# Kernel tuning notes

Measured on AMD Instinct MI355X. Metric: run time of the kernel, lower is better.

Reference implementation:

```python
import jax, jax.numpy as jnp
import numpy as np

N_HEADS = 4
D_HEAD = 32  # out_features // n_heads = 128 // 4
NEG_SLOPE = 0.2


def setup_inputs() -> dict:
    key = jax.random.key(0)
    k_x, k_adj, k_w, k_a = jax.random.split(key, 4)
    B, N, F_in, F_out = 4, 2048, 128, 128
    x = jax.random.normal(k_x, (B, N, F_in), dtype=jnp.float32)
    adj = jax.random.randint(k_adj, (B, N, N), 0, 2, dtype=jnp.int32)
    # Linear weight stored as [in, out] (torch stores [out, in]; math identical: x @ W)
    w_scale = np.sqrt(2.0 / (F_in + F_out))  # xavier-ish
    W = jax.random.normal(k_w, (F_in, F_out), dtype=jnp.float32) * w_scale
    a = jax.random.normal(k_a, (N_HEADS, 2 * D_HEAD), dtype=jnp.float32) * np.sqrt(2.0 / (2 * D_HEAD))
    return {"x": x, "adj": adj, "W": W, "a": a}


def reference(x, adj, W, a):
    B, N, _ = x.shape
    # project and split heads: [B, H, N, D]
    h = jnp.einsum('bnf,fo->bno', x, W).reshape(B, N, N_HEADS, D_HEAD).transpose(0, 2, 1, 3)
    # additive attention logits
    e_src = jnp.einsum('bhnd,hd->bhn', h, a[:, :D_HEAD])  # [B,H,N]
    e_dst = jnp.einsum('bhnd,hd->bhn', h, a[:, D_HEAD:])  # [B,H,N]
    e = e_src[:, :, :, None] + e_dst[:, :, None, :]       # [B,H,N,N]
    e = jnp.where(e > 0, e, NEG_SLOPE * e)                # leaky_relu(0.2)
    mask = (adj[:, None, :, :] == 0)                      # [B,1,N,N] -> broadcast over heads
    e = jnp.where(mask, -jnp.inf, e)
    alpha = jax.nn.softmax(e, axis=-1)                    # dropout omitted (eval mode)
    out = jnp.einsum('bhnm,bhmd->bhnd', alpha, h)         # weighted aggregation
    out = out.transpose(0, 2, 1, 3).reshape(B, N, N_HEADS * D_HEAD)
    return jax.nn.elu(out)
```

## Files before the change

kernel.cpp:

```cpp
#include <hip/hip_runtime.h>
#include <hip/hip_bf16.h>

#define BB 4
#define NN 2048
#define FIN 128
#define NH 4
#define DH 32
#define NS 0.2f

typedef unsigned int u32;
typedef unsigned short u16;
typedef unsigned long long u64;
typedef __attribute__((ext_vector_type(8))) short short8;
typedef __attribute__((ext_vector_type(4))) float f32x4;
typedef __attribute__((ext_vector_type(4))) unsigned int u32x4;

#define OFF_ES 0
#define OFF_ED 32768
#define OFF_PQ 65536
#define OFF_M  131072
#define OFF_HT 131088
#define OFF_BITS 655376

__device__ __forceinline__ u16 f2bf_rne(float f) {
  unsigned u = __float_as_uint(f);
  return (u16)((u + 0x7fffu + ((u >> 16) & 1u)) >> 16);
}

__device__ __forceinline__ int sign_bit(u32 w, int e) {
#if __has_builtin(__builtin_amdgcn_sbfe)
  return __builtin_amdgcn_sbfe((int)w, e, 1);
#else
  return ((int)(w << (31 - e))) >> 31;
#endif
}

__global__ __launch_bounds__(256) void k_pack(const int* __restrict__ adj,
                                              u32* __restrict__ bits) {
  const int row = (blockIdx.x << 2) | (threadIdx.x >> 6);
  const int lane = threadIdx.x & 63;
  const int* src = adj + (size_t)row * NN;
  u32* dst = bits + (size_t)row * 64;
#pragma unroll 8
  for (int it = 0; it < 32; ++it) {
    const int v = src[it * 64 + lane];
    const u64 m = __ballot(v != 0);
    if (lane == 0) *(u64*)(dst + it * 2) = m;
  }
}

__global__ __launch_bounds__(256) void k_proj(
    const float* __restrict__ x, const float* __restrict__ W,
    const float* __restrict__ a, u16* __restrict__ hT,
    float* __restrict__ e_src, float* __restrict__ e_dst) {
  __shared__ float Ws[FIN * 128];
  const int tid = threadIdx.x;
  const int f = tid & 127, g = tid >> 7;
  const float4* Wg4 = (const float4*)W;
  float4* Ws4 = (float4*)Ws;
#pragma unroll
  for (int t = 0; t < 16; ++t) Ws4[t * 256 + tid] = Wg4[t * 256 + tid];
  __syncthreads();

  const int rb = blockIdx.x * 16 + g * 8;
  const int head = f >> 5, d = f & 31;
  const int b = rb >> 11, n0 = rb & (NN - 1);
  const int bh = b * NH + head;
  const float a_s = a[head * (2 * DH) + d];
  const float a_d = a[head * (2 * DH) + DH + d];

  float acc[8];
#pragma unroll
  for (int r = 0; r < 8; ++r) acc[r] = 0.f;

  const float* xb = x + (size_t)rb * FIN;
  for (int k = 0; k < FIN; ++k) {
    const float wv = Ws[k * 128 + f];
#pragma unroll
    for (int r = 0; r < 8; ++r) acc[r] = fmaf(wv, xb[r * FIN + k], acc[r]);
  }

  u16 hs[8];
#pragma unroll
  for (int r = 0; r < 8; ++r) hs[r] = f2bf_rne(acc[r]);
  u16* dst = hT + ((size_t)bh * DH + d) * NN + n0;
  *(int4*)dst = *(int4*)&hs[0];

#pragma unroll
  for (int r = 0; r < 8; ++r) {
    float s1 = acc[r] * a_s;
    float s2 = acc[r] * a_d;
#pragma unroll
    for (int off = 16; off >= 1; off >>= 1) {
      s1 += __shfl_xor(s1, off);
      s2 += __shfl_xor(s2, off);
    }
    if (d == 0) {
      e_src[(size_t)bh * NN + n0 + r] = s1;
      e_dst[(size_t)bh * NN + n0 + r] = s2;
    }
  }
}

__global__ __launch_bounds__(64) void k_prep(
    const float* __restrict__ e_dst, u32* __restrict__ PQ,
    float* __restrict__ M) {
  const int bh = blockIdx.x >> 3, seg = blockIdx.x & 7;
  const int lane = threadIdx.x;
  const float* ed = e_dst + (size_t)bh * NN;
  float m = -1e30f;
#pragma unroll
  for (int t = 0; t < 32; ++t) m = fmaxf(m, ed[t * 64 + lane]);
#pragma unroll
  for (int off = 32; off >= 1; off >>= 1) m = fmaxf(m, __shfl_xor(m, off));
  if (seg == 0 && lane == 0) M[bh] = m;
#pragma unroll
  for (int t = 0; t < 4; ++t) {
    const int j = seg * 256 + t * 64 + lane;
    const float e = ed[j];
    const u32 pb = f2bf_rne(__expf(e));
    const u32 qb = f2bf_rne(__expf(NS * e));
    PQ[(size_t)bh * NN + j] = (qb << 16) | pb;
  }
}

__global__ __launch_bounds__(256) void k_attn(
    const u16* __restrict__ hT, const float* __restrict__ e_src,
    const u32* __restrict__ PQv, const float* __restrict__ Mv,
    const u32* __restrict__ bits, float* __restrict__ out) {
  __shared__ float part[4][32][33];
  __shared__ float sp[4][2][16];

  const int bid = blockIdx.x;
  const int bh = bid >> 6;
  const int it = bid & 63;
  const int b = bh >> 2, head = bh & 3;

  const int w = threadIdx.x >> 6;
  const int lane = threadIdx.x & 63;
  const int lg = lane >> 4, lm = lane & 15;

  const int i0 = it * 32 + lm;
  const int i1 = i0 + 16;
  const float m = Mv[bh];
  const float es0 = e_src[(size_t)bh * NN + i0];
  const float es1 = e_src[(size_t)bh * NN + i1];
  const float mr0 = es0 + m, mr1 = es1 + m;
  const float mi0 = fmaxf(mr0, NS * mr0), mi1 = fmaxf(mr1, NS * mr1);
  const float A0 = __expf(es0 - mi0), B0 = __expf(NS * es0 - mi0);
  const float A1 = __expf(es1 - mi1), B1 = __expf(NS * es1 - mi1);

  const u32* PQb = PQv + (size_t)bh * NN;
  const u16* hb0 = hT + ((size_t)bh * DH + lm) * NN;
  const u16* hb1 = hT + ((size_t)bh * DH + 16 + lm) * NN;
  const u32* br0 = bits + ((size_t)b * NN + i0) * 64 + w * 16;
  const u32* br1 = bits + ((size_t)b * NN + i1) * 64 + w * 16;
  const int shamt = lg * 8;

  u32 wd0[16], wd1[16];
#pragma unroll
  for (int jo = 0; jo < 4; ++jo) {
    const u32x4 v0 = *(const u32x4*)(br0 + jo * 4);
    const u32x4 v1 = *(const u32x4*)(br1 + jo * 4);
#pragma unroll
    for (int k = 0; k < 4; ++k) { wd0[jo * 4 + k] = v0[k]; wd1[jo * 4 + k] = v1[k]; }
  }

  f32x4 acc00 = {0,0,0,0}, acc01 = {0,0,0,0};
  f32x4 acc10 = {0,0,0,0}, acc11 = {0,0,0,0};
  float S0 = 0.f, S1 = 0.f;

  const int jbase = w * 512 + lg * 8;

  u32x4 pqa_c = *(const u32x4*)(PQb + jbase);
  u32x4 pqb_c = *(const u32x4*)(PQb + jbase + 4);
  short8 h0_c = *(const short8*)(hb0 + jbase);
  short8 h1_c = *(const short8*)(hb1 + jbase);

#pragma unroll
  for (int c = 0; c < 16; ++c) {
    u32x4 pqa_n, pqb_n; short8 h0_n, h1_n;
    if (c < 15) {
      const int jn = jbase + (c + 1) * 32;
      pqa_n = *(const u32x4*)(PQb + jn);
      pqb_n = *(const u32x4*)(PQb + jn + 4);
      h0_n = *(const short8*)(hb0 + jn);
      h1_n = *(const short8*)(hb1 + jn);
    }
    const u32 wsh0 = wd0[c] >> shamt;
    const u32 wsh1 = wd1[c] >> shamt;
    short8 af0, af1;
#pragma unroll
    for (int e = 0; e < 8; ++e) {
      const u32 pq = (e < 4) ? pqa_c[e] : pqb_c[e - 4];
      const float Pf = __uint_as_float(pq << 16);
      const float Qf = __uint_as_float(pq & 0xffff0000u);
      const int m0 = sign_bit(wsh0, e);
      const int m1 = sign_bit(wsh1, e);
      float w0 = fmaxf(A0 * Pf, B0 * Qf);
      w0 = __int_as_float(__float_as_int(w0) & m0);
      S0 += w0;
      af0[e] = (short)__builtin_bit_cast(unsigned short, __float2bfloat16(w0));
      float w1 = fmaxf(A1 * Pf, B1 * Qf);
      w1 = __int_as_float(__float_as_int(w1) & m1);
      S1 += w1;
      af1[e] = (short)__builtin_bit_cast(unsigned short, __float2bfloat16(w1));
    }
    __builtin_amdgcn_s_setprio(1);
    acc00 = __builtin_amdgcn_mfma_f32_16x16x32_bf16(af0, h0_c, acc00, 0, 0, 0);
    acc01 = __builtin_amdgcn_mfma_f32_16x16x32_bf16(af0, h1_c, acc01, 0, 0, 0);
    acc10 = __builtin_amdgcn_mfma_f32_16x16x32_bf16(af1, h0_c, acc10, 0, 0, 0);
    acc11 = __builtin_amdgcn_mfma_f32_16x16x32_bf16(af1, h1_c, acc11, 0, 0, 0);
    __builtin_amdgcn_s_setprio(0);
    if (c < 15) { pqa_c = pqa_n; pqb_c = pqb_n; h0_c = h0_n; h1_c = h1_n; }
  }

  S0 += __shfl_xor(S0, 16); S0 += __shfl_xor(S0, 32);
  S1 += __shfl_xor(S1, 16); S1 += __shfl_xor(S1, 32);

#pragma unroll
  for (int r = 0; r < 4; ++r) {
    const int rl = lg * 4 + r;
    part[w][rl][lm] = acc00[r];
    part[w][rl][16 + lm] = acc01[r];
    part[w][16 + rl][lm] = acc10[r];
    part[w][16 + rl][16 + lm] = acc11[r];
  }
  if (lg == 0) { sp[w][0][lm] = S0; sp[w][1][lm] = S1; }
  __syncthreads();

  const int tid = threadIdx.x;
#pragma unroll
  for (int t = 0; t < 4; ++t) {
    const int idx = t * 256 + tid;
    const int row = idx >> 5, d = idx & 31;
    const float v = part[0][row][d] + part[1][row][d] +
                    part[2][row][d] + part[3][row][d];
    const float s = sp[0][row >> 4][row & 15] + sp[1][row >> 4][row & 15] +
                    sp[2][row >> 4][row & 15] + sp[3][row >> 4][row & 15];
    const float o = v / s;
    const int n = it * 32 + row;
    out[((size_t)b * NN + n) * 128 + head * 32 + d] =
        o > 0.f ? o : (__expf(o) - 1.f);
  }
}

extern "C" void kernel_launch(void* const* d_in, const int* in_sizes, int n_in,
                              void* d_out, int out_size, void* d_ws, size_t ws_size,
                              hipStream_t stream) {
  const float* x = (const float*)d_in[0];
  const int* adj = (const int*)d_in[1];
  const float* W = (const float*)d_in[2];
  const float* a = (const float*)d_in[3];
  float* out = (float*)d_out;
  float* ws = (float*)d_ws;

  float* e_src = ws + OFF_ES;
  float* e_dst = ws + OFF_ED;
  u32* PQv = (u32*)(ws + OFF_PQ);
  float* Mv = ws + OFF_M;
  u16* hT = (u16*)(ws + OFF_HT);
  u32* bits = (u32*)(ws + OFF_BITS);

  k_pack<<<(BB * NN) / 4, 256, 0, stream>>>(adj, bits);
  k_proj<<<(BB * NN) / 16, 256, 0, stream>>>(x, W, a, hT, e_src, e_dst);
  k_prep<<<BB * NH * 8, 64, 0, stream>>>(e_dst, PQv, Mv);
  k_attn<<<BB * NH * 64, 256, 0, stream>>>(hT, e_src, PQv, Mv, bits, out);
}
```

Baseline: 64.79 us.

## Stage hT tiles through swizzled LDS with per-wave double buffering in attention kernel

The attention kernel no longer has each lane read strided 16-byte chunks of h^T straight from global memory. Each wave now loads 32x64 tiles of h^T with coalesced row reads, writes them into an XOR-swizzled LDS double buffer, and reads the MFMA B operands from LDS. The adjacency bit words are loaded per stage instead of being preloaded into 32 registers, and the part/sp reduction buffers reuse the same LDS after a barrier. This is meant to improve global coalescing and cut register pressure, at the cost of extra LDS traffic and no explicit intra-wave sync between the LDS writes and reads.

Measured after the change: 62.43 us. -3.6%, faster.

```diff
diff --git a/kernel.cpp b/kernel.cpp
--- a/kernel.cpp
+++ b/kernel.cpp
@@ -25,14 +25,6 @@
 __device__ __forceinline__ u16 f2bf_rne(float f) {
   unsigned u = __float_as_uint(f);
   return (u16)((u + 0x7fffu + ((u >> 16) & 1u)) >> 16);
-}
-
-__device__ __forceinline__ int sign_bit(u32 w, int e) {
-#if __has_builtin(__builtin_amdgcn_sbfe)
-  return __builtin_amdgcn_sbfe((int)w, e, 1);
-#else
-  return ((int)(w << (31 - e))) >> 31;
-#endif
 }
 
 __global__ __launch_bounds__(256) void k_pack(const int* __restrict__ adj,
@@ -128,8 +120,7 @@
     const u16* __restrict__ hT, const float* __restrict__ e_src,
     const u32* __restrict__ PQv, const float* __restrict__ Mv,
     const u32* __restrict__ bits, float* __restrict__ out) {
-  __shared__ float part[4][32][33];
-  __shared__ float sp[4][2][16];
+  __shared__ __align__(16) u16 smem[4][2][32 * 64];
 
   const int bid = blockIdx.x;
   const int bh = bid >> 6;
@@ -150,73 +141,96 @@
   const float A0 = __expf(es0 - mi0), B0 = __expf(NS * es0 - mi0);
   const float A1 = __expf(es1 - mi1), B1 = __expf(NS * es1 - mi1);
 
-  const u32* PQb = PQv + (size_t)bh * NN;
-  const u16* hb0 = hT + ((size_t)bh * DH + lm) * NN;
-  const u16* hb1 = hT + ((size_t)bh * DH + 16 + lm) * NN;
+  const u32* PQb = PQv + (size_t)bh * NN + w * 512;
+  const u16* hb = hT + (size_t)bh * DH * NN + w * 512;
   const u32* br0 = bits + ((size_t)b * NN + i0) * 64 + w * 16;
   const u32* br1 = bits + ((size_t)b * NN + i1) * 64 + w * 16;
   const int shamt = lg * 8;
 
-  u32 wd0[16], wd1[16];
-#pragma unroll
-  for (int jo = 0; jo < 4; ++jo) {
-    const u32x4 v0 = *(const u32x4*)(br0 + jo * 4);
-    const u32x4 v1 = *(const u32x4*)(br1 + jo * 4);
-#pragma unroll
-    for (int k = 0; k < 4; ++k) { wd0[jo * 4 + k] = v0[k]; wd1[jo * 4 + k] = v1[k]; }
-  }
+  const int sd = lane >> 3;
+  const int sj = (lane & 7) * 8;
+  u16* stg0 = &smem[w][0][0];
+  u16* stg1 = &smem[w][1][0];
+  const int woff = (sd * 64 + sj) ^ (sd << 3);
 
   f32x4 acc00 = {0,0,0,0}, acc01 = {0,0,0,0};
   f32x4 acc10 = {0,0,0,0}, acc11 = {0,0,0,0};
   float S0 = 0.f, S1 = 0.f;
 
-  const int jbase = w * 512 + lg * 8;
-
-  u32x4 pqa_c = *(const u32x4*)(PQb + jbase);
-  u32x4 pqb_c = *(const u32x4*)(PQb + jbase + 4);
-  short8 h0_c = *(const short8*)(hb0 + jbase);
-  short8 h1_c = *(const short8*)(hb1 + jbase);
-
-#pragma unroll
-  for (int c = 0; c < 16; ++c) {
-    u32x4 pqa_n, pqb_n; short8 h0_n, h1_n;
-    if (c < 15) {
-      const int jn = jbase + (c + 1) * 32;
-      pqa_n = *(const u32x4*)(PQb + jn);
-      pqb_n = *(const u32x4*)(PQb + jn + 4);
-      h0_n = *(const short8*)(hb0 + jn);
-      h1_n = *(const short8*)(hb1 + jn);
-    }
-    const u32 wsh0 = wd0[c] >> shamt;
-    const u32 wsh1 = wd1[c] >> shamt;
-    short8 af0, af1;
-#pragma unroll
-    for (int e = 0; e < 8; ++e) {
-      const u32 pq = (e < 4) ? pqa_c[e] : pqb_c[e - 4];
-      const float Pf = __uint_as_float(pq << 16);
-      const float Qf = __uint_as_float(pq & 0xffff0000u);
-      const int m0 = sign_bit(wsh0, e);
-      const int m1 = sign_bit(wsh1, e);
-      float w0 = fmaxf(A0 * Pf, B0 * Qf);
-      w0 = __int_as_float(__float_as_int(w0) & m0);
-      S0 += w0;
-      af0[e] = (short)__builtin_bit_cast(unsigned short, __float2bfloat16(w0));
-      float w1 = fmaxf(A1 * Pf, B1 * Qf);
-      w1 = __int_as_float(__float_as_int(w1) & m1);
-      S1 += w1;
-      af1[e] = (short)__builtin_bit_cast(unsigned short, __float2bfloat16(w1));
-    }
-    __builtin_amdgcn_s_setprio(1);
-    acc00 = __builtin_amdgcn_mfma_f32_16x16x32_bf16(af0, h0_c, acc00, 0, 0, 0);
-    acc01 = __builtin_amdgcn_mfma_f32_16x16x32_bf16(af0, h1_c, acc01, 0, 0, 0);
-    acc10 = __builtin_amdgcn_mfma_f32_16x16x32_bf16(af1, h0_c, acc10, 0, 0, 0);
-    acc11 = __builtin_amdgcn_mfma_f32_16x16x32_bf16(af1, h1_c, acc11, 0, 0, 0);
-    __builtin_amdgcn_s_setprio(0);
-    if (c < 15) { pqa_c = pqa_n; pqb_c = pqb_n; h0_c = h0_n; h1_c = h1_n; }
+  {
+    int4 r0 = *(const int4*)(hb + (size_t)(0 * 8 + sd) * NN + sj);
+    int4 r1 = *(const int4*)(hb + (size_t)(1 * 8 + sd) * NN + sj);
+    int4 r2 = *(const int4*)(hb + (size_t)(2 * 8 + sd) * NN + sj);
+    int4 r3 = *(const int4*)(hb + (size_t)(3 * 8 + sd) * NN + sj);
+    *(int4*)(stg0 + woff) = r0;
+    *(int4*)(stg0 + woff + 1 * 512) = r1;
+    *(int4*)(stg0 + woff + 2 * 512) = r2;
+    *(int4*)(stg0 + woff + 3 * 512) = r3;
+  }
+
+  const int ra0 = (lm * 64) ^ ((lm & 7) << 3);
+
+#pragma unroll
+  for (int s = 0; s < 8; ++s) {
+    u16* cur = (s & 1) ? stg1 : stg0;
+    u16* nxt = (s & 1) ? stg0 : stg1;
+    int4 n0, n1, n2, n3;
+    if (s < 7) {
+      const u16* g = hb + (s + 1) * 64;
+      n0 = *(const int4*)(g + (size_t)(0 * 8 + sd) * NN + sj);
+      n1 = *(const int4*)(g + (size_t)(1 * 8 + sd) * NN + sj);
+      n2 = *(const int4*)(g + (size_t)(2 * 8 + sd) * NN + sj);
+      n3 = *(const int4*)(g + (size_t)(3 * 8 + sd) * NN + sj);
+    }
+    const u64 wb0 = *(const u64*)(br0 + s * 2);
+    const u64 wb1 = *(const u64*)(br1 + s * 2);
+#pragma unroll
+    for (int c = 0; c < 2; ++c) {
+      const int jl = c * 32 + lg * 8;
+      const u32x4 pqa = *(const u32x4*)(PQb + s * 64 + jl);
+      const u32x4 pqb = *(const u32x4*)(PQb + s * 64 + jl + 4);
+      const short8 hv0 = *(const short8*)(cur + (ra0 ^ jl));
+      const short8 hv1 = *(const short8*)(cur + ((ra0 ^ jl) + 16 * 64));
+      const u32 wsh0 = ((u32)(wb0 >> (c * 32))) >> shamt;
+      const u32 wsh1 = ((u32)(wb1 >> (c * 32))) >> shamt;
+      short8 af0, af1;
+#pragma unroll
+      for (int e = 0; e < 8; ++e) {
+        const u32 pq = (e < 4) ? pqa[e] : pqb[e - 4];
+        const float Pf = __uint_as_float(pq << 16);
+        const float Qf = __uint_as_float(pq & 0xffff0000u);
+        const int m0 = ((int)(wsh0 << (31 - e))) >> 31;
+        const int m1 = ((int)(wsh1 << (31 - e))) >> 31;
+        float w0 = fmaxf(A0 * Pf, B0 * Qf);
+        w0 = __int_as_float(__float_as_int(w0) & m0);
+        S0 += w0;
+        af0[e] = (short)__builtin_bit_cast(unsigned short, __float2bfloat16(w0));
+        float w1 = fmaxf(A1 * Pf, B1 * Qf);
+        w1 = __int_as_float(__float_as_int(w1) & m1);
+        S1 += w1;
+        af1[e] = (short)__builtin_bit_cast(unsigned short, __float2bfloat16(w1));
+      }
+      __builtin_amdgcn_s_setprio(1);
+      acc00 = __builtin_amdgcn_mfma_f32_16x16x32_bf16(af0, hv0, acc00, 0, 0, 0);
+      acc01 = __builtin_amdgcn_mfma_f32_16x16x32_bf16(af0, hv1, acc01, 0, 0, 0);
+      acc10 = __builtin_amdgcn_mfma_f32_16x16x32_bf16(af1, hv0, acc10, 0, 0, 0);
+      acc11 = __builtin_amdgcn_mfma_f32_16x16x32_bf16(af1, hv1, acc11, 0, 0, 0);
+      __builtin_amdgcn_s_setprio(0);
+    }
+    if (s < 7) {
+      *(int4*)(nxt + woff) = n0;
+      *(int4*)(nxt + woff + 1 * 512) = n1;
+      *(int4*)(nxt + woff + 2 * 512) = n2;
+      *(int4*)(nxt + woff + 3 * 512) = n3;
+    }
   }
 
   S0 += __shfl_xor(S0, 16); S0 += __shfl_xor(S0, 32);
   S1 += __shfl_xor(S1, 16); S1 += __shfl_xor(S1, 32);
+
+  __syncthreads();
+  float (*part)[32][33] = (float (*)[32][33]) & smem[0][0][0];
+  float (*sp)[2][16] = (float (*)[2][16])((char*)&smem[0][0][0] + 16896);
 
 #pragma unroll
   for (int r = 0; r < 4; ++r) {
```
